# Performance work log

Measured on AMD Instinct MI355X. Metric: run time of the kernel, lower is better.

The kernel has to match this reference:

```python
import jax, jax.numpy as jnp
import numpy as np

N_NODES = 50000
N_EDGES = 625000
DIM = 128
DROPOUT_P = 0.5


def setup_inputs() -> dict:
    key = jax.random.key(0)
    kx, ke, kw, kb = jax.random.split(key, 4)
    x = jax.random.normal(kx, (N_NODES, DIM), dtype=jnp.float32)
    edge_index = jax.random.randint(ke, (2, N_EDGES), 0, N_NODES, dtype=jnp.int64)
    # GCNConv linear weight (glorot-ish) and bias
    W = jax.random.normal(kw, (DIM, DIM), dtype=jnp.float32) / np.sqrt(DIM)
    b = jnp.zeros((DIM,), dtype=jnp.float32)
    return {"x": x, "edge_index": edge_index, "W": W, "b": b}


def reference(x, edge_index, W, b):
    N = x.shape[0]
    # --- add self-loops ---
    loop = jnp.arange(N, dtype=edge_index.dtype)
    src = jnp.concatenate([edge_index[0], loop])  # [E+N]
    dst = jnp.concatenate([edge_index[1], loop])  # [E+N]
    # --- symmetric normalization: deg computed on destination nodes ---
    deg = jax.ops.segment_sum(jnp.ones_like(src, dtype=x.dtype), dst, num_segments=N)
    dis = jnp.where(deg > 0, jax.lax.rsqrt(jnp.where(deg > 0, deg, 1.0)), 0.0)
    norm = dis[src] * dis[dst]  # [E+N]
    # --- linear transform, gather, scatter-add ---
    h = x @ W  # [N, D]
    msg = h[src] * norm[:, None]  # [E+N, D]
    out = jax.ops.segment_sum(msg, dst, num_segments=N) + b  # [N, D]
    # --- ReLU + dropout (training mode, fixed key) + residual ---
    out = jax.nn.relu(out)
    keep = jax.random.bernoulli(jax.random.key(42), 1.0 - DROPOUT_P, out.shape)
    out = jnp.where(keep, out / (1.0 - DROPOUT_P), 0.0)
    out = out + x  # residual: input_dim == output_dim
    return out
```

## Files before the change

### kernel.cpp

```cpp
#include <hip/hip_runtime.h>
#include <hip/hip_bf16.h>
#include <stdint.h>

#define NDIM 128
#define LDK 136
#define BSH 9
#define NB_A 1024
#define BCAP 9216

typedef __attribute__((ext_vector_type(8))) short bf16x8;
typedef __attribute__((ext_vector_type(4))) float f32x4;

__device__ __forceinline__ unsigned short f2bf(float f) {
    unsigned u = __float_as_uint(f);
    unsigned r = u + 0x7fffu + ((u >> 16) & 1u);
    return (unsigned short)(r >> 16);
}
__device__ __forceinline__ float bf2f(unsigned short s) {
    return __uint_as_float(((unsigned)s) << 16);
}

__device__ __forceinline__ void load_edge(const unsigned* __restrict__ w, int is64, int E,
                                          int e, int& s, int& d) {
    if (is64) {
        s = (int)w[(size_t)2 * e];
        d = (int)w[(size_t)2 * E + (size_t)2 * e];
    } else {
        s = (int)w[e];
        d = (int)w[(size_t)E + e];
    }
}

__device__ __forceinline__ int detect_is64(const unsigned* __restrict__ w,
                                           int lo, int hi, int E, int t, int* nzflag) {
    if (t == 0) *nzflag = 0;
    __syncthreads();
    int k = lo + t;
    if (k < hi && w[2 * (size_t)k + 1] != 0u) atomicOr(nzflag, 1);
    __syncthreads();
    return *nzflag ? 0 : 1;
}

__global__ __launch_bounds__(256) void hist_kernel(const unsigned* __restrict__ w,
                                                   const float* __restrict__ W,
                                                   unsigned short* __restrict__ WbfT,
                                                   int* __restrict__ hist,
                                                   int* __restrict__ lock,
                                                   int E, int nbuck, int chunk) {
    __shared__ int h[128];
    __shared__ int nzflag;
    int t = threadIdx.x;
    if (t < 128) h[t] = 0;
    if (t == 0 && blockIdx.x == 0) *lock = 0;
    int lo = blockIdx.x * chunk;
    int hi = lo + chunk; if (hi > E) hi = E;
    int is64 = detect_is64(w, lo, hi, E, t, &nzflag);

    if (blockIdx.x < 64) {
        int idx = blockIdx.x * 256 + t;
        int k = idx >> 7, c = idx & 127;
        WbfT[c * 128 + k] = f2bf(W[idx]);
    }

    for (int e = lo + t; e < hi; e += 256) {
        int s, d; load_edge(w, is64, E, e, s, d);
        atomicAdd(&h[d >> BSH], 1);
    }
    __syncthreads();
    if (t < nbuck) hist[(size_t)t * gridDim.x + blockIdx.x] = h[t];
}

__global__ __launch_bounds__(1024) void scanhist_kernel(int* __restrict__ hist,
                                                        int* __restrict__ btot,
                                                        int* __restrict__ bbase,
                                                        int* __restrict__ off,
                                                        int* __restrict__ lock,
                                                        int NB, int nbuck, int N, int E) {
    __shared__ int s[1024];
    __shared__ int amlast;
    int t = threadIdx.x;
    if (t == 0) amlast = 0;
    size_t base = (size_t)blockIdx.x * NB;
    int v = hist[base + t];
    s[t] = v;
    __syncthreads();
    for (int d = 1; d < 1024; d <<= 1) {
        int add = (t >= d) ? s[t - d] : 0;
        __syncthreads();
        s[t] += add;
        __syncthreads();
    }
    hist[base + t] = s[t] - v;
    if (t == 1023) {
        atomicExch(&btot[blockIdx.x], s[1023]);
        __threadfence();
        int prev = atomicAdd(lock, 1);
        amlast = (prev == nbuck - 1) ? 1 : 0;
    }
    __syncthreads();
    if (amlast) {
        int v2 = (t < nbuck) ? atomicAdd(&btot[t], 0) : 0;
        s[t] = v2;
        __syncthreads();
        for (int d = 1; d < 128; d <<= 1) {
            int add = (t >= d && t < 128) ? s[t - d] : 0;
            __syncthreads();
            if (t < 128) s[t] += add;
            __syncthreads();
        }
        if (t < nbuck) bbase[t] = s[t] - v2;
        if (t == 0) off[N] = E;
    }
}

__global__ __launch_bounds__(256) void bucket_kernel(const unsigned* __restrict__ w,
                                                     const int* __restrict__ hist,
                                                     const int* __restrict__ bbase,
                                                     unsigned* __restrict__ ebuf,
                                                     int E, int nbuck, int chunk) {
    __shared__ int cur[128];
    __shared__ int nzflag;
    int t = threadIdx.x;
    if (t < nbuck) cur[t] = bbase[t] + hist[(size_t)t * gridDim.x + blockIdx.x];
    int lo = blockIdx.x * chunk;
    int hi = lo + chunk; if (hi > E) hi = E;
    int is64 = detect_is64(w, lo, hi, E, t, &nzflag);
    for (int e = lo + t; e < hi; e += 256) {
        int s, d; load_edge(w, is64, E, e, s, d);
        int b = d >> BSH;
        int p = atomicAdd(&cur[b], 1);
        ebuf[p] = ((unsigned)s << BSH) | (unsigned)(d & ((1 << BSH) - 1));
    }
}

__global__ __launch_bounds__(512) void csr_kernel(const unsigned* __restrict__ ebuf,
                                                  const int* __restrict__ bbase,
                                                  const int* __restrict__ btot,
                                                  int* __restrict__ adj,
                                                  int* __restrict__ off,
                                                  float* __restrict__ dis,
                                                  int N) {
    __shared__ int lcnt[512];
    __shared__ int lscan[512];
    __shared__ int cur[512];
    __shared__ int tile[BCAP];
    int b = blockIdx.x, t = threadIdx.x;
    int start = bbase[b], cnt = btot[b];
    lcnt[t] = 0;
    __syncthreads();
    for (int i = t; i < cnt; i += 512) atomicAdd(&lcnt[ebuf[start + i] & 511], 1);
    __syncthreads();
    int v = lcnt[t];
    lscan[t] = v;
    __syncthreads();
    for (int d = 1; d < 512; d <<= 1) {
        int add = (t >= d) ? lscan[t - d] : 0;
        __syncthreads();
        lscan[t] += add;
        __syncthreads();
    }
    int ex = lscan[t] - v;
    int node = (b << BSH) + t;
    if (node < N) {
        off[node] = start + ex;
        dis[node] = rsqrtf((float)(v + 1));
    }
    cur[t] = ex;
    __syncthreads();
    if (cnt <= BCAP) {
        for (int i = t; i < cnt; i += 512) {
            unsigned wo = ebuf[start + i];
            int p = atomicAdd(&cur[wo & 511], 1);
            tile[p] = (int)(wo >> BSH);
        }
        __syncthreads();
        for (int i = t; i < cnt; i += 512) adj[start + i] = tile[i];
    } else {
        for (int i = t; i < cnt; i += 512) {
            unsigned wo = ebuf[start + i];
            int p = atomicAdd(&cur[wo & 511], 1);
            adj[start + p] = (int)(wo >> BSH);
        }
    }
}

__global__ __launch_bounds__(256) void gemm_kernel(const float* __restrict__ x,
                                                   const unsigned short* __restrict__ WbfT,
                                                   const float* __restrict__ dis,
                                                   unsigned short* __restrict__ hp, int N) {
    __shared__ unsigned short Wt[NDIM][LDK];
    int tid = threadIdx.x;
    for (int ch = tid; ch < 2048; ch += 256) {
        int c = ch >> 4;
        int k8 = (ch & 15) << 3;
        bf16x8 v = *(const bf16x8*)(WbfT + c * 128 + k8);
        *(bf16x8*)&Wt[c][k8] = v;
    }
    __syncthreads();

    const int lane = tid & 63;
    const int wv = tid >> 6;
    const int rowbase = blockIdx.x * 64 + wv * 16;
    const int l15 = lane & 15;
    const int kg = lane >> 4;
    const int arow = rowbase + l15;

    bf16x8 a[4];
#pragma unroll
    for (int s = 0; s < 4; ++s) {
        bf16x8 tt;
        if (arow < N) {
            const float* p = x + (size_t)arow * NDIM + s * 32 + kg * 8;
            float4 f0 = *(const float4*)p;
            float4 f1 = *(const float4*)(p + 4);
            tt[0] = (short)f2bf(f0.x); tt[1] = (short)f2bf(f0.y);
            tt[2] = (short)f2bf(f0.z); tt[3] = (short)f2bf(f0.w);
            tt[4] = (short)f2bf(f1.x); tt[5] = (short)f2bf(f1.y);
            tt[6] = (short)f2bf(f1.z); tt[7] = (short)f2bf(f1.w);
        } else {
#pragma unroll
            for (int e = 0; e < 8; ++e) tt[e] = 0;
        }
        a[s] = tt;
    }

    f32x4 acc[8];
#pragma unroll
    for (int ct = 0; ct < 8; ++ct) acc[ct] = (f32x4){0.f, 0.f, 0.f, 0.f};

#pragma unroll
    for (int ct = 0; ct < 8; ++ct) {
#pragma unroll
        for (int s = 0; s < 4; ++s) {
            bf16x8 bb = *(const bf16x8*)&Wt[ct * 16 + l15][s * 32 + kg * 8];
            acc[ct] = __builtin_amdgcn_mfma_f32_16x16x32_bf16(a[s], bb, acc[ct], 0, 0, 0);
        }
    }

    const int r0 = rowbase + kg * 4;
    float dv[4];
#pragma unroll
    for (int j = 0; j < 4; ++j) dv[j] = (r0 + j < N) ? dis[r0 + j] : 0.f;
#pragma unroll
    for (int ct = 0; ct < 8; ++ct) {
        int col = ct * 16 + l15;
#pragma unroll
        for (int j = 0; j < 4; ++j) {
            int r = r0 + j;
            if (r < N) hp[(size_t)r * NDIM + col] = f2bf(acc[ct][j] * dv[j]);
        }
    }
}

__device__ __forceinline__ unsigned rotl32(unsigned v, int d) {
    return (v << d) | (v >> (32 - d));
}
__device__ __forceinline__ unsigned tf_bits(unsigned ctr) {
    unsigned x0 = 0u, x1 = ctr;
    const unsigned ks0 = 0u, ks1 = 42u, ks2 = 0u ^ 42u ^ 0x1BD11BDAu;
    x0 += ks0; x1 += ks1;
#define RND(r) { x0 += x1; x1 = rotl32(x1, (r)); x1 ^= x0; }
    RND(13) RND(15) RND(26) RND(6)   x0 += ks1; x1 += ks2 + 1u;
    RND(17) RND(29) RND(16) RND(24)  x0 += ks2; x1 += ks0 + 2u;
    RND(13) RND(15) RND(26) RND(6)   x0 += ks0; x1 += ks1 + 3u;
    RND(17) RND(29) RND(16) RND(24)  x0 += ks1; x1 += ks2 + 4u;
    RND(13) RND(15) RND(26) RND(6)   x0 += ks2; x1 += ks0 + 5u;
#undef RND
    return x0 ^ x1;
}

__global__ __launch_bounds__(256) void gather_kernel(const unsigned short* __restrict__ hp,
                                                     const float* __restrict__ x,
                                                     const int* __restrict__ off,
                                                     const int* __restrict__ adj,
                                                     const float* __restrict__ dis,
                                                     const float* __restrict__ b,
                                                     float* __restrict__ out, int N) {
    int wid = (int)((blockIdx.x * 256u + threadIdx.x) >> 6);
    int lane = threadIdx.x & 63;
    int half = lane >> 5;
    int l32 = lane & 31;
    int node = wid * 2 + half;
    bool valid = node < N;
    int nodec = valid ? node : N - 1;
    const float dn = dis[nodec];
    const int c0 = l32 * 4;
    const unsigned short* hpc = hp + c0;

    unsigned ctr = (unsigned)(nodec * NDIM + c0);
    unsigned bt0 = tf_bits(ctr);
    unsigned bt1 = tf_bits(ctr + 1u);
    unsigned bt2 = tf_bits(ctr + 2u);
    unsigned bt3 = tf_bits(ctr + 3u);

    uint2 hv = *(const uint2*)(hpc + (size_t)nodec * NDIM);
    float a00 = bf2f((unsigned short)hv.x), a01 = bf2f((unsigned short)(hv.x >> 16));
    float a02 = bf2f((unsigned short)hv.y), a03 = bf2f((unsigned short)(hv.y >> 16));
    float a10 = 0.f, a11 = 0.f, a12 = 0.f, a13 = 0.f;
    float a20 = 0.f, a21 = 0.f, a22 = 0.f, a23 = 0.f;
    float a30 = 0.f, a31 = 0.f, a32 = 0.f, a33 = 0.f;

    int k0 = valid ? off[nodec] : 0;
    int k1 = valid ? off[nodec + 1] : 0;
    int kb = k0;
    const int sbase = half << 5;
    while (kb < k1) {
        int nb = k1 - kb; if (nb > 32) nb = 32;
        int myadj = (kb + l32 < k1) ? adj[kb + l32] : 0;
        int j = 0;
        for (; j + 8 <= nb; j += 8) {
            int s0 = __shfl(myadj, sbase + j);
            int s1 = __shfl(myadj, sbase + j + 1);
            int s2 = __shfl(myadj, sbase + j + 2);
            int s3 = __shfl(myadj, sbase + j + 3);
            int s4 = __shfl(myadj, sbase + j + 4);
            int s5 = __shfl(myadj, sbase + j + 5);
            int s6 = __shfl(myadj, sbase + j + 6);
            int s7 = __shfl(myadj, sbase + j + 7);
            uint2 v0 = *(const uint2*)(hpc + (size_t)s0 * NDIM);
            uint2 v1 = *(const uint2*)(hpc + (size_t)s1 * NDIM);
            uint2 v2 = *(const uint2*)(hpc + (size_t)s2 * NDIM);
            uint2 v3 = *(const uint2*)(hpc + (size_t)s3 * NDIM);
            uint2 v4 = *(const uint2*)(hpc + (size_t)s4 * NDIM);
            uint2 v5 = *(const uint2*)(hpc + (size_t)s5 * NDIM);
            uint2 v6 = *(const uint2*)(hpc + (size_t)s6 * NDIM);
            uint2 v7 = *(const uint2*)(hpc + (size_t)s7 * NDIM);
            a00 += bf2f((unsigned short)v0.x); a01 += bf2f((unsigned short)(v0.x >> 16));
            a02 += bf2f((unsigned short)v0.y); a03 += bf2f((unsigned short)(v0.y >> 16));
            a10 += bf2f((unsigned short)v1.x); a11 += bf2f((unsigned short)(v1.x >> 16));
            a12 += bf2f((unsigned short)v1.y); a13 += bf2f((unsigned short)(v1.y >> 16));
            a20 += bf2f((unsigned short)v2.x); a21 += bf2f((unsigned short)(v2.x >> 16));
            a22 += bf2f((unsigned short)v2.y); a23 += bf2f((unsigned short)(v2.y >> 16));
            a30 += bf2f((unsigned short)v3.x); a31 += bf2f((unsigned short)(v3.x >> 16));
            a32 += bf2f((unsigned short)v3.y); a33 += bf2f((unsigned short)(v3.y >> 16));
            a00 += bf2f((unsigned short)v4.x); a01 += bf2f((unsigned short)(v4.x >> 16));
            a02 += bf2f((unsigned short)v4.y); a03 += bf2f((unsigned short)(v4.y >> 16));
            a10 += bf2f((unsigned short)v5.x); a11 += bf2f((unsigned short)(v5.x >> 16));
            a12 += bf2f((unsigned short)v5.y); a13 += bf2f((unsigned short)(v5.y >> 16));
            a20 += bf2f((unsigned short)v6.x); a21 += bf2f((unsigned short)(v6.x >> 16));
            a22 += bf2f((unsigned short)v6.y); a23 += bf2f((unsigned short)(v6.y >> 16));
            a30 += bf2f((unsigned short)v7.x); a31 += bf2f((unsigned short)(v7.x >> 16));
            a32 += bf2f((unsigned short)v7.y); a33 += bf2f((unsigned short)(v7.y >> 16));
        }
        if (j + 4 <= nb) {
            int s0 = __shfl(myadj, sbase + j);
            int s1 = __shfl(myadj, sbase + j + 1);
            int s2 = __shfl(myadj, sbase + j + 2);
            int s3 = __shfl(myadj, sbase + j + 3);
            uint2 v0 = *(const uint2*)(hpc + (size_t)s0 * NDIM);
            uint2 v1 = *(const uint2*)(hpc + (size_t)s1 * NDIM);
            uint2 v2 = *(const uint2*)(hpc + (size_t)s2 * NDIM);
            uint2 v3 = *(const uint2*)(hpc + (size_t)s3 * NDIM);
            a00 += bf2f((unsigned short)v0.x); a01 += bf2f((unsigned short)(v0.x >> 16));
            a02 += bf2f((unsigned short)v0.y); a03 += bf2f((unsigned short)(v0.y >> 16));
            a10 += bf2f((unsigned short)v1.x); a11 += bf2f((unsigned short)(v1.x >> 16));
            a12 += bf2f((unsigned short)v1.y); a13 += bf2f((unsigned short)(v1.y >> 16));
            a20 += bf2f((unsigned short)v2.x); a21 += bf2f((unsigned short)(v2.x >> 16));
            a22 += bf2f((unsigned short)v2.y); a23 += bf2f((unsigned short)(v2.y >> 16));
            a30 += bf2f((unsigned short)v3.x); a31 += bf2f((unsigned short)(v3.x >> 16));
            a32 += bf2f((unsigned short)v3.y); a33 += bf2f((unsigned short)(v3.y >> 16));
            j += 4;
        }
        for (; j < nb; ++j) {
            int s = __shfl(myadj, sbase + j);
            uint2 v = *(const uint2*)(hpc + (size_t)s * NDIM);
            a00 += bf2f((unsigned short)v.x); a01 += bf2f((unsigned short)(v.x >> 16));
            a02 += bf2f((unsigned short)v.y); a03 += bf2f((unsigned short)(v.y >> 16));
        }
        kb += nb;
    }

    float c0s = (a00 + a10) + (a20 + a30);
    float c1s = (a01 + a11) + (a21 + a31);
    float c2s = (a02 + a12) + (a22 + a32);
    float c3s = (a03 + a13) + (a23 + a33);

    float4 bb = *(const float4*)(b + c0);
    float v0 = fmaxf(fmaf(dn, c0s, bb.x), 0.f);
    float v1 = fmaxf(fmaf(dn, c1s, bb.y), 0.f);
    float v2 = fmaxf(fmaf(dn, c2s, bb.z), 0.f);
    float v3 = fmaxf(fmaf(dn, c3s, bb.w), 0.f);

    v0 = (bt0 >> 31) ? 0.f : v0 * 2.f;
    v1 = (bt1 >> 31) ? 0.f : v1 * 2.f;
    v2 = (bt2 >> 31) ? 0.f : v2 * 2.f;
    v3 = (bt3 >> 31) ? 0.f : v3 * 2.f;

    if (valid) {
        float4 xr = *(const float4*)(x + (size_t)node * NDIM + c0);
        float4 o;
        o.x = v0 + xr.x; o.y = v1 + xr.y; o.z = v2 + xr.z; o.w = v3 + xr.w;
        *(float4*)(out + (size_t)node * NDIM + c0) = o;
    }
}

extern "C" void kernel_launch(void* const* d_in, const int* in_sizes, int n_in,
                              void* d_out, int out_size, void* d_ws, size_t ws_size,
                              hipStream_t stream) {
    const float* x = (const float*)d_in[0];
    const unsigned* edge_w = (const unsigned*)d_in[1];
    const float* W = (const float*)d_in[2];
    const float* b = (const float*)d_in[3];
    float* out = (float*)d_out;

    const int N = in_sizes[0] / NDIM;
    const int E = in_sizes[1] / 2;
    const int nbuck = (N + (1 << BSH) - 1) >> BSH;
    const int chunk = (E + NB_A - 1) / NB_A;

    char* ws = (char*)d_ws;
    unsigned short* hp = (unsigned short*)ws;
    float* dis   = (float*)(ws + (size_t)N * NDIM * sizeof(short));
    int*   off   = (int*)((char*)dis + (size_t)N * sizeof(float));
    int*   adj   = (int*)((char*)off + (size_t)(N + 4) * sizeof(int));
    unsigned* ebuf = (unsigned*)((char*)adj + (size_t)E * sizeof(int));
    int*   hist  = (int*)((char*)ebuf + (size_t)E * sizeof(unsigned));
    int*   btot  = (int*)((char*)hist + (size_t)128 * NB_A * sizeof(int));
    int*   bbase = (int*)((char*)btot + (size_t)128 * sizeof(int));
    int*   lock  = (int*)((char*)bbase + (size_t)128 * sizeof(int));
    unsigned short* WbfT = (unsigned short*)((char*)lock + 64);

    hist_kernel<<<NB_A, 256, 0, stream>>>(edge_w, W, WbfT, hist, lock, E, nbuck, chunk);
    scanhist_kernel<<<nbuck, 1024, 0, stream>>>(hist, btot, bbase, off, lock, NB_A, nbuck, N, E);
    bucket_kernel<<<NB_A, 256, 0, stream>>>(edge_w, hist, bbase, ebuf, E, nbuck, chunk);
    csr_kernel<<<nbuck, 512, 0, stream>>>(ebuf, bbase, btot, adj, off, dis, N);

    gemm_kernel<<<(N + 63) / 64, 256, 0, stream>>>(x, WbfT, dis, hp, N);

    int waves = (N + 1) / 2;
    gather_kernel<<<(waves + 3) / 4, 256, 0, stream>>>(hp, x, off, adj, dis, b, out, N);
}
```

Baseline: 78.31 us.

## Fuse CSR build and GEMM into one launch, apply source norm in gather

Merges the CSR construction kernel and the bf16 MFMA GEMM into a single launch: the first blocks build the CSR and the rest compute h = x@W, sharing LDS through a union. Because the GEMM no longer depends on dis, the per-source normalization moves into the gather loop as an FMA using dis loaded per adjacency entry and broadcast with shuffles. This removes one kernel launch and lets the GEMM overlap with CSR building. In exchange the gather does extra dis loads and shuffles, and the 4-edge unrolled tail path is dropped.

```diff
diff --git a/kernel.cpp b/kernel.cpp
--- a/kernel.cpp
+++ b/kernel.cpp
@@ -32,7 +32,7 @@
 }
 
 __device__ __forceinline__ int detect_is64(const unsigned* __restrict__ w,
-                                           int lo, int hi, int E, int t, int* nzflag) {
+                                           int lo, int hi, int t, int* nzflag) {
     if (t == 0) *nzflag = 0;
     __syncthreads();
     int k = lo + t;
@@ -54,7 +54,7 @@
     if (t == 0 && blockIdx.x == 0) *lock = 0;
     int lo = blockIdx.x * chunk;
     int hi = lo + chunk; if (hi > E) hi = E;
-    int is64 = detect_is64(w, lo, hi, E, t, &nzflag);
+    int is64 = detect_is64(w, lo, hi, t, &nzflag);
 
     if (blockIdx.x < 64) {
         int idx = blockIdx.x * 256 + t;
@@ -124,130 +124,122 @@
     if (t < nbuck) cur[t] = bbase[t] + hist[(size_t)t * gridDim.x + blockIdx.x];
     int lo = blockIdx.x * chunk;
     int hi = lo + chunk; if (hi > E) hi = E;
-    int is64 = detect_is64(w, lo, hi, E, t, &nzflag);
+    int is64 = detect_is64(w, lo, hi, t, &nzflag);
     for (int e = lo + t; e < hi; e += 256) {
         int s, d; load_edge(w, is64, E, e, s, d);
         int b = d >> BSH;
         int p = atomicAdd(&cur[b], 1);
-        ebuf[p] = ((unsigned)s << BSH) | (unsigned)(d & ((1 << BSH) - 1));
-    }
-}
-
-__global__ __launch_bounds__(512) void csr_kernel(const unsigned* __restrict__ ebuf,
-                                                  const int* __restrict__ bbase,
-                                                  const int* __restrict__ btot,
-                                                  int* __restrict__ adj,
-                                                  int* __restrict__ off,
-                                                  float* __restrict__ dis,
-                                                  int N) {
-    __shared__ int lcnt[512];
-    __shared__ int lscan[512];
-    __shared__ int cur[512];
-    __shared__ int tile[BCAP];
-    int b = blockIdx.x, t = threadIdx.x;
-    int start = bbase[b], cnt = btot[b];
-    lcnt[t] = 0;
-    __syncthreads();
-    for (int i = t; i < cnt; i += 512) atomicAdd(&lcnt[ebuf[start + i] & 511], 1);
-    __syncthreads();
-    int v = lcnt[t];
-    lscan[t] = v;
-    __syncthreads();
-    for (int d = 1; d < 512; d <<= 1) {
-        int add = (t >= d) ? lscan[t - d] : 0;
-        __syncthreads();
-        lscan[t] += add;
-        __syncthreads();
-    }
-    int ex = lscan[t] - v;
-    int node = (b << BSH) + t;
-    if (node < N) {
-        off[node] = start + ex;
-        dis[node] = rsqrtf((float)(v + 1));
-    }
-    cur[t] = ex;
-    __syncthreads();
-    if (cnt <= BCAP) {
-        for (int i = t; i < cnt; i += 512) {
-            unsigned wo = ebuf[start + i];
-            int p = atomicAdd(&cur[wo & 511], 1);
-            tile[p] = (int)(wo >> BSH);
-        }
-        __syncthreads();
-        for (int i = t; i < cnt; i += 512) adj[start + i] = tile[i];
+        ebuf[p] = ((unsigned)s << BSH) | (unsigned)(d & 511);
+    }
+}
+
+__global__ __launch_bounds__(512) void csrgemm_kernel(const unsigned* __restrict__ ebuf,
+                                                      const int* __restrict__ bbase,
+                                                      const int* __restrict__ btot,
+                                                      int* __restrict__ adj,
+                                                      int* __restrict__ off,
+                                                      float* __restrict__ dis,
+                                                      const float* __restrict__ x,
+                                                      const unsigned short* __restrict__ WbfT,
+                                                      unsigned short* __restrict__ hp,
+                                                      int N, int nbuck) {
+    __shared__ union {
+        struct { int lcnt[512]; int lscan[512]; int cur[512]; int tile[BCAP]; } cs;
+        unsigned short Wt[NDIM][LDK];
+    } u;
+    int t = threadIdx.x;
+    if (blockIdx.x < nbuck) {
+        int b = blockIdx.x;
+        int start = bbase[b], cnt = btot[b];
+        u.cs.lcnt[t] = 0;
+        __syncthreads();
+        for (int i = t; i < cnt; i += 512) atomicAdd(&u.cs.lcnt[ebuf[start + i] & 511], 1);
+        __syncthreads();
+        int v = u.cs.lcnt[t];
+        u.cs.lscan[t] = v;
+        __syncthreads();
+        for (int d = 1; d < 512; d <<= 1) {
+            int add = (t >= d) ? u.cs.lscan[t - d] : 0;
+            __syncthreads();
+            u.cs.lscan[t] += add;
+            __syncthreads();
+        }
+        int ex = u.cs.lscan[t] - v;
+        int node = (b << BSH) + t;
+        if (node < N) {
+            off[node] = start + ex;
+            dis[node] = rsqrtf((float)(v + 1));
+        }
+        u.cs.cur[t] = ex;
+        __syncthreads();
+        if (cnt <= BCAP) {
+            for (int i = t; i < cnt; i += 512) {
+                unsigned wo = ebuf[start + i];
+                int p = atomicAdd(&u.cs.cur[wo & 511], 1);
+                u.cs.tile[p] = (int)(wo >> BSH);
+            }
+            __syncthreads();
+            for (int i = t; i < cnt; i += 512) adj[start + i] = u.cs.tile[i];
+        } else {
+            for (int i = t; i < cnt; i += 512) {
+                unsigned wo = ebuf[start + i];
+                int p = atomicAdd(&u.cs.cur[wo & 511], 1);
+                adj[start + p] = (int)(wo >> BSH);
+            }
+        }
     } else {
-        for (int i = t; i < cnt; i += 512) {
-            unsigned wo = ebuf[start + i];
-            int p = atomicAdd(&cur[wo & 511], 1);
-            adj[start + p] = (int)(wo >> BSH);
-        }
-    }
-}
-
-__global__ __launch_bounds__(256) void gemm_kernel(const float* __restrict__ x,
-                                                   const unsigned short* __restrict__ WbfT,
-                                                   const float* __restrict__ dis,
-                                                   unsigned short* __restrict__ hp, int N) {
-    __shared__ unsigned short Wt[NDIM][LDK];
-    int tid = threadIdx.x;
-    for (int ch = tid; ch < 2048; ch += 256) {
-        int c = ch >> 4;
-        int k8 = (ch & 15) << 3;
-        bf16x8 v = *(const bf16x8*)(WbfT + c * 128 + k8);
-        *(bf16x8*)&Wt[c][k8] = v;
-    }
-    __syncthreads();
-
-    const int lane = tid & 63;
-    const int wv = tid >> 6;
-    const int rowbase = blockIdx.x * 64 + wv * 16;
-    const int l15 = lane & 15;
-    const int kg = lane >> 4;
-    const int arow = rowbase + l15;
-
-    bf16x8 a[4];
-#pragma unroll
-    for (int s = 0; s < 4; ++s) {
-        bf16x8 tt;
-        if (arow < N) {
-            const float* p = x + (size_t)arow * NDIM + s * 32 + kg * 8;
-            float4 f0 = *(const float4*)p;
-            float4 f1 = *(const float4*)(p + 4);
-            tt[0] = (short)f2bf(f0.x); tt[1] = (short)f2bf(f0.y);
-            tt[2] = (short)f2bf(f0.z); tt[3] = (short)f2bf(f0.w);
-            tt[4] = (short)f2bf(f1.x); tt[5] = (short)f2bf(f1.y);
-            tt[6] = (short)f2bf(f1.z); tt[7] = (short)f2bf(f1.w);
-        } else {
-#pragma unroll
-            for (int e = 0; e < 8; ++e) tt[e] = 0;
-        }
-        a[s] = tt;
-    }
-
-    f32x4 acc[8];
-#pragma unroll
-    for (int ct = 0; ct < 8; ++ct) acc[ct] = (f32x4){0.f, 0.f, 0.f, 0.f};
-
-#pragma unroll
-    for (int ct = 0; ct < 8; ++ct) {
+        for (int ch = t; ch < 2048; ch += 512) {
+            int c = ch >> 4, k8 = (ch & 15) << 3;
+            *(bf16x8*)&u.Wt[c][k8] = *(const bf16x8*)(WbfT + c * 128 + k8);
+        }
+        __syncthreads();
+        const int lane = t & 63;
+        const int wv = t >> 6;
+        const int l15 = lane & 15;
+        const int kg = lane >> 4;
+        const int rowbase = (blockIdx.x - nbuck) * 128 + wv * 16;
+        const int arow = rowbase + l15;
+
+        bf16x8 a[4];
 #pragma unroll
         for (int s = 0; s < 4; ++s) {
-            bf16x8 bb = *(const bf16x8*)&Wt[ct * 16 + l15][s * 32 + kg * 8];
-            acc[ct] = __builtin_amdgcn_mfma_f32_16x16x32_bf16(a[s], bb, acc[ct], 0, 0, 0);
-        }
-    }
-
-    const int r0 = rowbase + kg * 4;
-    float dv[4];
-#pragma unroll
-    for (int j = 0; j < 4; ++j) dv[j] = (r0 + j < N) ? dis[r0 + j] : 0.f;
-#pragma unroll
-    for (int ct = 0; ct < 8; ++ct) {
-        int col = ct * 16 + l15;
-#pragma unroll
-        for (int j = 0; j < 4; ++j) {
-            int r = r0 + j;
-            if (r < N) hp[(size_t)r * NDIM + col] = f2bf(acc[ct][j] * dv[j]);
+            bf16x8 tt;
+            if (arow < N) {
+                const float* p = x + (size_t)arow * NDIM + s * 32 + kg * 8;
+                float4 f0 = *(const float4*)p;
+                float4 f1 = *(const float4*)(p + 4);
+                tt[0] = (short)f2bf(f0.x); tt[1] = (short)f2bf(f0.y);
+                tt[2] = (short)f2bf(f0.z); tt[3] = (short)f2bf(f0.w);
+                tt[4] = (short)f2bf(f1.x); tt[5] = (short)f2bf(f1.y);
+                tt[6] = (short)f2bf(f1.z); tt[7] = (short)f2bf(f1.w);
+            } else {
+#pragma unroll
+                for (int e = 0; e < 8; ++e) tt[e] = 0;
+            }
+            a[s] = tt;
+        }
+
+        f32x4 acc[8];
+#pragma unroll
+        for (int ct = 0; ct < 8; ++ct) acc[ct] = (f32x4){0.f, 0.f, 0.f, 0.f};
+#pragma unroll
+        for (int ct = 0; ct < 8; ++ct) {
+#pragma unroll
+            for (int s = 0; s < 4; ++s) {
+                bf16x8 bb = *(const bf16x8*)&u.Wt[ct * 16 + l15][s * 32 + kg * 8];
+                acc[ct] = __builtin_amdgcn_mfma_f32_16x16x32_bf16(a[s], bb, acc[ct], 0, 0, 0);
+            }
+        }
+
+        const int r0 = rowbase + kg * 4;
+#pragma unroll
+        for (int ct = 0; ct < 8; ++ct) {
+            int col = ct * 16 + l15;
+#pragma unroll
+            for (int j = 0; j < 4; ++j) {
+                int r = r0 + j;
+                if (r < N) hp[(size_t)r * NDIM + col] = f2bf(acc[ct][j]);
+            }
         }
     }
 }
@@ -294,8 +286,8 @@
     unsigned bt3 = tf_bits(ctr + 3u);
 
     uint2 hv = *(const uint2*)(hpc + (size_t)nodec * NDIM);
-    float a00 = bf2f((unsigned short)hv.x), a01 = bf2f((unsigned short)(hv.x >> 16));
-    float a02 = bf2f((unsigned short)hv.y), a03 = bf2f((unsigned short)(hv.y >> 16));
+    float a00 = bf2f((unsigned short)hv.x) * dn, a01 = bf2f((unsigned short)(hv.x >> 16)) * dn;
+    float a02 = bf2f((unsigned short)hv.y) * dn, a03 = bf2f((unsigned short)(hv.y >> 16)) * dn;
     float a10 = 0.f, a11 = 0.f, a12 = 0.f, a13 = 0.f;
     float a20 = 0.f, a21 = 0.f, a22 = 0.f, a23 = 0.f;
     float a30 = 0.f, a31 = 0.f, a32 = 0.f, a33 = 0.f;
@@ -307,6 +299,7 @@
     while (kb < k1) {
         int nb = k1 - kb; if (nb > 32) nb = 32;
         int myadj = (kb + l32 < k1) ? adj[kb + l32] : 0;
+        float mydis = dis[myadj];
         int j = 0;
         for (; j + 8 <= nb; j += 8) {
             int s0 = __shfl(myadj, sbase + j);
@@ -325,47 +318,55 @@
             uint2 v5 = *(const uint2*)(hpc + (size_t)s5 * NDIM);
             uint2 v6 = *(const uint2*)(hpc + (size_t)s6 * NDIM);
             uint2 v7 = *(const uint2*)(hpc + (size_t)s7 * NDIM);
-            a00 += bf2f((unsigned short)v0.x); a01 += bf2f((unsigned short)(v0.x >> 16));
-            a02 += bf2f((unsigned short)v0.y); a03 += bf2f((unsigned short)(v0.y >> 16));
-            a10 += bf2f((unsigned short)v1.x); a11 += bf2f((unsigned short)(v1.x >> 16));
-            a12 += bf2f((unsigned short)v1.y); a13 += bf2f((unsigned short)(v1.y >> 16));
-            a20 += bf2f((unsigned short)v2.x); a21 += bf2f((unsigned short)(v2.x >> 16));
-            a22 += bf2f((unsigned short)v2.y); a23 += bf2f((unsigned short)(v2.y >> 16));
-            a30 += bf2f((unsigned short)v3.x); a31 += bf2f((unsigned short)(v3.x >> 16));
-            a32 += bf2f((unsigned short)v3.y); a33 += bf2f((unsigned short)(v3.y >> 16));
-            a00 += bf2f((unsigned short)v4.x); a01 += bf2f((unsigned short)(v4.x >> 16));
-            a02 += bf2f((unsigned short)v4.y); a03 += bf2f((unsigned short)(v4.y >> 16));
-            a10 += bf2f((unsigned short)v5.x); a11 += bf2f((unsigned short)(v5.x >> 16));
-            a12 += bf2f((unsigned short)v5.y); a13 += bf2f((unsigned short)(v5.y >> 16));
-            a20 += bf2f((unsigned short)v6.x); a21 += bf2f((unsigned short)(v6.x >> 16));
-            a22 += bf2f((unsigned short)v6.y); a23 += bf2f((unsigned short)(v6.y >> 16));
-            a30 += bf2f((unsigned short)v7.x); a31 += bf2f((unsigned short)(v7.x >> 16));
-            a32 += bf2f((unsigned short)v7.y); a33 += bf2f((unsigned short)(v7.y >> 16));
-        }
-        if (j + 4 <= nb) {
-            int s0 = __shfl(myadj, sbase + j);
-            int s1 = __shfl(myadj, sbase + j + 1);
-            int s2 = __shfl(myadj, sbase + j + 2);
-            int s3 = __shfl(myadj, sbase + j + 3);
-            uint2 v0 = *(const uint2*)(hpc + (size_t)s0 * NDIM);
-            uint2 v1 = *(const uint2*)(hpc + (size_t)s1 * NDIM);
-            uint2 v2 = *(const uint2*)(hpc + (size_t)s2 * NDIM);
-            uint2 v3 = *(const uint2*)(hpc + (size_t)s3 * NDIM);
-            a00 += bf2f((unsigned short)v0.x); a01 += bf2f((unsigned short)(v0.x >> 16));
-            a02 += bf2f((unsigned short)v0.y); a03 += bf2f((unsigned short)(v0.y >> 16));
-            a10 += bf2f((unsigned short)v1.x); a11 += bf2f((unsigned short)(v1.x >> 16));
-            a12 += bf2f((unsigned short)v1.y); a13 += bf2f((unsigned short)(v1.y >> 16));
-            a20 += bf2f((unsigned short)v2.x); a21 += bf2f((unsigned short)(v2.x >> 16));
-            a22 += bf2f((unsigned short)v2.y); a23 += bf2f((unsigned short)(v2.y >> 16));
-            a30 += bf2f((unsigned short)v3.x); a31 += bf2f((unsigned short)(v3.x >> 16));
-            a32 += bf2f((unsigned short)v3.y); a33 += bf2f((unsigned short)(v3.y >> 16));
-            j += 4;
+            float n0 = __shfl(mydis, sbase + j);
+            float n1 = __shfl(mydis, sbase + j + 1);
+            float n2 = __shfl(mydis, sbase + j + 2);
+            float n3 = __shfl(mydis, sbase + j + 3);
+            float n4 = __shfl(mydis, sbase + j + 4);
+            float n5 = __shfl(mydis, sbase + j + 5);
+            float n6 = __shfl(mydis, sbase + j + 6);
+            float n7 = __shfl(mydis, sbase + j + 7);
+            a00 = fmaf(bf2f((unsigned short)v0.x), n0, a00);
+            a01 = fmaf(bf2f((unsigned short)(v0.x >> 16)), n0, a01);
+            a02 = fmaf(bf2f((unsigned short)v0.y), n0, a02);
+            a03 = fmaf(bf2f((unsigned short)(v0.y >> 16)), n0, a03);
+            a10 = fmaf(bf2f((unsigned short)v1.x), n1, a10);
+            a11 = fmaf(bf2f((unsigned short)(v1.x >> 16)), n1, a11);
+            a12 = fmaf(bf2f((unsigned short)v1.y), n1, a12);
+            a13 = fmaf(bf2f((unsigned short)(v1.y >> 16)), n1, a13);
+            a20 = fmaf(bf2f((unsigned short)v2.x), n2, a20);
+            a21 = fmaf(bf2f((unsigned short)(v2.x >> 16)), n2, a21);
+            a22 = fmaf(bf2f((unsigned short)v2.y), n2, a22);
+            a23 = fmaf(bf2f((unsigned short)(v2.y >> 16)), n2, a23);
+            a30 = fmaf(bf2f((unsigned short)v3.x), n3, a30);
+            a31 = fmaf(bf2f((unsigned short)(v3.x >> 16)), n3, a31);
+            a32 = fmaf(bf2f((unsigned short)v3.y), n3, a32);
+            a33 = fmaf(bf2f((unsigned short)(v3.y >> 16)), n3, a33);
+            a00 = fmaf(bf2f((unsigned short)v4.x), n4, a00);
+            a01 = fmaf(bf2f((unsigned short)(v4.x >> 16)), n4, a01);
+            a02 = fmaf(bf2f((unsigned short)v4.y), n4, a02);
+            a03 = fmaf(bf2f((unsigned short)(v4.y >> 16)), n4, a03);
+            a10 = fmaf(bf2f((unsigned short)v5.x), n5, a10);
+            a11 = fmaf(bf2f((unsigned short)(v5.x >> 16)), n5, a11);
+            a12 = fmaf(bf2f((unsigned short)v5.y), n5, a12);
+            a13 = fmaf(bf2f((unsigned short)(v5.y >> 16)), n5, a13);
+            a20 = fmaf(bf2f((unsigned short)v6.x), n6, a20);
+            a21 = fmaf(bf2f((unsigned short)(v6.x >> 16)), n6, a21);
+            a22 = fmaf(bf2f((unsigned short)v6.y), n6, a22);
+            a23 = fmaf(bf2f((unsigned short)(v6.y >> 16)), n6, a23);
+            a30 = fmaf(bf2f((unsigned short)v7.x), n7, a30);
+            a31 = fmaf(bf2f((unsigned short)(v7.x >> 16)), n7, a31);
+            a32 = fmaf(bf2f((unsigned short)v7.y), n7, a32);
+            a33 = fmaf(bf2f((unsigned short)(v7.y >> 16)), n7, a33);
         }
         for (; j < nb; ++j) {
             int s = __shfl(myadj, sbase + j);
+            float nn = __shfl(mydis, sbase + j);
             uint2 v = *(const uint2*)(hpc + (size_t)s * NDIM);
-            a00 += bf2f((unsigned short)v.x); a01 += bf2f((unsigned short)(v.x >> 16));
-            a02 += bf2f((unsigned short)v.y); a03 += bf2f((unsigned short)(v.y >> 16));
+            a00 = fmaf(bf2f((unsigned short)v.x), nn, a00);
+            a01 = fmaf(bf2f((unsigned short)(v.x >> 16)), nn, a01);
+            a02 = fmaf(bf2f((unsigned short)v.y), nn, a02);
+            a03 = fmaf(bf2f((unsigned short)(v.y >> 16)), nn, a03);
         }
         kb += nb;
     }
@@ -407,6 +408,7 @@
     const int E = in_sizes[1] / 2;
     const int nbuck = (N + (1 << BSH) - 1) >> BSH;
     const int chunk = (E + NB_A - 1) / NB_A;
+    const int ntiles = (N + 127) / 128;
 
     char* ws = (char*)d_ws;
     unsigned short* hp = (unsigned short*)ws;
@@ -423,9 +425,8 @@
     hist_kernel<<<NB_A, 256, 0, stream>>>(edge_w, W, WbfT, hist, lock, E, nbuck, chunk);
     scanhist_kernel<<<nbuck, 1024, 0, stream>>>(hist, btot, bbase, off, lock, NB_A, nbuck, N, E);
     bucket_kernel<<<NB_A, 256, 0, stream>>>(edge_w, hist, bbase, ebuf, E, nbuck, chunk);
-    csr_kernel<<<nbuck, 512, 0, stream>>>(ebuf, bbase, btot, adj, off, dis, N);
-
-    gemm_kernel<<<(N + 63) / 64, 256, 0, stream>>>(x, WbfT, dis, hp, N);
+    csrgemm_kernel<<<nbuck + ntiles, 512, 0, stream>>>(ebuf, bbase, btot, adj, off, dis,
+                                                       x, WbfT, hp, N, nbuck);
 
     int waves = (N + 1) / 2;
     gather_kernel<<<(waves + 3) / 4, 256, 0, stream>>>(hp, x, off, adj, dis, b, out, N);
```

Result: faster. 74.02 us, median of 2 (-5.5%).
